# Kernel optimization log

Hardware: AMD Instinct MI355X
Metric: run time of the kernel (lower is better)

## Reference

```python
import jax, jax.numpy as jnp
import numpy as np

N = 100000   # nodes
E = 640000   # edges
H = 8        # attention heads
C = 16       # hidden_channels (per-head out dim)
IN = 4       # in_channels
G = 64       # graphs in the batch
NE = 2       # num_experts
HC = H * C   # 128 = concat feature width
SLOPE = 0.2  # GATConv leaky_relu negative slope


def _p(k, shape):
    return 0.1 * jax.random.normal(k, shape, jnp.float32)


def setup_inputs() -> dict:
    key = jax.random.key(0)
    ks = jax.random.split(key, 32)
    inp = {
        "x": jax.random.normal(ks[0], (N, IN), jnp.float32),
        "edge_index": jax.random.randint(ks[1], (2, E), 0, N),
        "edge_attr": jax.random.normal(ks[2], (E, 1), jnp.float32),
        "batch": jnp.sort(jax.random.randint(ks[3], (N,), 0, G)),
    }
    i = 4
    for l, d in zip((1, 2, 3), (IN, HC, HC)):
        inp[f"w{l}"] = _p(ks[i], (d, HC)); i += 1      # node lin
        inp[f"as{l}"] = _p(ks[i], (H, C)); i += 1      # att_src
        inp[f"ad{l}"] = _p(ks[i], (H, C)); i += 1      # att_dst
        inp[f"we{l}"] = _p(ks[i], (1, HC)); i += 1     # lin_edge
        inp[f"ae{l}"] = _p(ks[i], (H, C)); i += 1      # att_edge
        inp[f"b{l}"] = jnp.zeros((HC,), jnp.float32)
    inp["fw1"] = _p(ks[i], (HC, 4 * C)); inp["fb1"] = jnp.zeros((4 * C,), jnp.float32)
    inp["fw2"] = _p(ks[i + 1], (4 * C, NE)); inp["fb2"] = jnp.zeros((NE,), jnp.float32)
    return inp


def gat_layer(x, src, dst, eattr, w, a_s, a_d, we, a_e, b):
    """PyG GATConv (concat=True, edge_dim=1): gather-attend-segment_softmax-scatter."""
    n = x.shape[0]
    h = (x @ w).reshape(n, H, C)                       # [N,H,C]
    alpha_src = jnp.sum(h * a_s, axis=-1)              # [N,H]
    alpha_dst = jnp.sum(h * a_d, axis=-1)              # [N,H]
    ef = (eattr @ we).reshape(-1, H, C)                # [E,H,C]
    alpha_e = jnp.sum(ef * a_e, axis=-1)               # [E,H]
    alpha = jax.nn.leaky_relu(alpha_src[src] + alpha_dst[dst] + alpha_e, SLOPE)
    # segment softmax over incoming edges of each dst node
    m = jax.lax.stop_gradient(jax.ops.segment_max(alpha, dst, num_segments=n))
    m = jnp.where(jnp.isfinite(m), m, 0.0)
    ex = jnp.exp(alpha - m[dst])
    den = jax.ops.segment_sum(ex, dst, num_segments=n)
    alpha = ex / (den[dst] + 1e-16)
    out = jax.ops.segment_sum(h[src] * alpha[:, :, None], dst, num_segments=n)
    return out.reshape(n, HC) + b


def add_self_loops_mean(src, dst, eattr, n):
    """add_self_loops(fill_value='mean'): self-loop attr = mean of incoming edge attrs."""
    cnt = jax.ops.segment_sum(jnp.ones(src.shape, eattr.dtype), dst, num_segments=n)
    loop = jax.ops.segment_sum(eattr, dst, num_segments=n) / jnp.maximum(cnt, 1.0)[:, None]
    idx = jnp.arange(n, dtype=src.dtype)
    return (jnp.concatenate([src, idx]), jnp.concatenate([dst, idx]),
            jnp.concatenate([eattr, loop], axis=0))


def reference(x, edge_index, edge_attr, batch,
              w1, as1, ad1, we1, ae1, b1,
              w2, as2, ad2, we2, ae2, b2,
              w3, as3, ad3, we3, ae3, b3,
              fw1, fb1, fw2, fb2):
    src, dst = edge_index[0], edge_index[1]
    # conv1: add_self_loops=False
    h = jax.nn.relu(gat_layer(x, src, dst, edge_attr, w1, as1, ad1, we1, ae1, b1))
    # conv2/conv3: default add_self_loops=True with fill_value='mean'
    s2, d2, e2 = add_self_loops_mean(src, dst, edge_attr, x.shape[0])
    h = jax.nn.relu(gat_layer(h, s2, d2, e2, w2, as2, ad2, we2, ae2, b2))
    h = jax.nn.relu(gat_layer(h, s2, d2, e2, w3, as3, ad3, we3, ae3, b3))
    # global mean pool over `batch`
    gsum = jax.ops.segment_sum(h, batch, num_segments=G)
    cnt = jax.ops.segment_sum(jnp.ones((h.shape[0],), h.dtype), batch, num_segments=G)
    emb = gsum / jnp.maximum(cnt, 1.0)[:, None]
    gh = jax.nn.relu(emb @ fw1 + fb1)
    return gh @ fw2 + fb2
```

## Files before the change

### kernel.cpp

```cpp
#include <hip/hip_runtime.h>
#include <hip/hip_bf16.h>
#include <math.h>

#define NHEAD 8
#define CDIM 16
#define HCDIM 128
#define NGRAPH 64
#define WEXT 144
#define SWPAD 136

typedef __attribute__((ext_vector_type(8))) short short8;
typedef __attribute__((ext_vector_type(4))) float f32x4;
typedef __attribute__((ext_vector_type(2))) float f32x2;

static __device__ __forceinline__ unsigned short f2bf(float f) {
    unsigned u = __float_as_uint(f);
    unsigned r = (u + 0x7FFF + ((u >> 16) & 1)) >> 16;
    return (unsigned short)r;
}
static __device__ __forceinline__ float bf2f(unsigned short s) {
    return __uint_as_float(((unsigned)s) << 16);
}
static __device__ __forceinline__ unsigned char f2fp8(float v) {
    int r = __builtin_amdgcn_cvt_pk_fp8_f32(v, v, 0, false);
    return (unsigned char)(r & 0xff);
}


__global__ void setup0(int* __restrict__ deg,
                       float* __restrict__ gsum,
                       const float* __restrict__ w2, const float* __restrict__ w3,
                       unsigned short* __restrict__ wt2, unsigned short* __restrict__ wt3,
                       const float* __restrict__ we1, const float* __restrict__ ae1,
                       const float* __restrict__ we2, const float* __restrict__ ae2,
                       const float* __restrict__ we3, const float* __restrict__ ae3,
                       float* __restrict__ kc,
                       const float* __restrict__ as2, const float* __restrict__ ad2,
                       const float* __restrict__ as3, const float* __restrict__ ad3,
                       const float* __restrict__ w1,
                       const float* __restrict__ as1, const float* __restrict__ ad1,
                       float* __restrict__ wastab, float* __restrict__ wadtab,
                       const int* __restrict__ batch, int* __restrict__ gstart, int n) {
    int i = blockIdx.x * 256 + threadIdx.x;
    if (i < n) deg[i] = 0;
    if (i < NGRAPH * HCDIM) gsum[i] = 0.f;
    if (i < WEXT * HCDIM) {
        int nn = i >> 7, k = i & 127;
        float v2, v3;
        if (nn < HCDIM) {
            v2 = w2[k * HCDIM + nn];
            v3 = w3[k * HCDIM + nn];
        } else if (nn < HCDIM + NHEAD) {
            int h = nn - HCDIM;
            float s2 = 0.f, s3 = 0.f;
#pragma unroll
            for (int c = 0; c < CDIM; ++c) {
                s2 += w2[k * HCDIM + h * CDIM + c] * as2[h * CDIM + c];
                s3 += w3[k * HCDIM + h * CDIM + c] * as3[h * CDIM + c];
            }
            v2 = s2; v3 = s3;
        } else {
            int h = nn - HCDIM - NHEAD;
            float s2 = 0.f, s3 = 0.f;
#pragma unroll
            for (int c = 0; c < CDIM; ++c) {
                s2 += w2[k * HCDIM + h * CDIM + c] * ad2[h * CDIM + c];
                s3 += w3[k * HCDIM + h * CDIM + c] * ad3[h * CDIM + c];
            }
            v2 = s2; v3 = s3;
        }
        wt2[nn * HCDIM + k] = f2bf(v2);
        wt3[nn * HCDIM + k] = f2bf(v3);
    }
    if (i < 24) {
        int l = i >> 3, h = i & 7;
        const float* we = (l == 0) ? we1 : ((l == 1) ? we2 : we3);
        const float* ae = (l == 0) ? ae1 : ((l == 1) ? ae2 : ae3);
        float s = 0.f;
        for (int c = 0; c < CDIM; ++c) s += we[h * CDIM + c] * ae[h * CDIM + c];
        kc[i] = s;
    }
    if (i >= 18560 && i <= 18560 + NGRAPH) {
        int g = i - 18560;
        int lo = 0, hi = n;
        while (lo < hi) {
            int mid = (lo + hi) >> 1;
            if (batch[mid] < g) lo = mid + 1; else hi = mid;
        }
        gstart[g] = lo;
    }
    if (i >= 18700 && i < 18732) {
        int t = i - 18700;
        int k = t >> 3, h = t & 7;
        float ss = 0.f, sd = 0.f;
#pragma unroll
        for (int c = 0; c < CDIM; ++c) {
            ss += w1[k * HCDIM + h * CDIM + c] * as1[h * CDIM + c];
            sd += w1[k * HCDIM + h * CDIM + c] * ad1[h * CDIM + c];
        }
        wastab[t] = ss;
        wadtab[t] = sd;
    }
}

__global__ void count_deg(const int* __restrict__ dst, int* __restrict__ deg,
                          int* __restrict__ erank, int E) {
    int e = blockIdx.x * 256 + threadIdx.x;
    if (e >= E) return;
    erank[e] = atomicAdd(&deg[dst[e]], 1);
}

__global__ __launch_bounds__(512) void block_sum(const int* __restrict__ deg,
                                                 int* __restrict__ bsum, int n) {
    __shared__ int s[512];
    int i = blockIdx.x * 512 + threadIdx.x;
    s[threadIdx.x] = (i < n) ? deg[i] : 0;
    __syncthreads();
    for (int off = 256; off > 0; off >>= 1) {
        if (threadIdx.x < off) s[threadIdx.x] += s[threadIdx.x + off];
        __syncthreads();
    }
    if (threadIdx.x == 0) bsum[blockIdx.x] = s[0];
}

__global__ __launch_bounds__(512) void scan_final2(const int* __restrict__ deg,
                                                   const int* __restrict__ bsum, int nb,
                                                   int* __restrict__ eoff, int n) {
    __shared__ int ls[512];
    __shared__ int s[512];
    const int t = threadIdx.x;
    ls[t] = (t < nb) ? bsum[t] : 0;
    int i = blockIdx.x * 512 + t;
    s[t] = (i < n) ? deg[i] : 0;
    __syncthreads();
    for (int off = 1; off < 512; off <<= 1) {
        int a1 = (t >= off) ? ls[t - off] : 0;
        int a2 = (t >= off) ? s[t - off] : 0;
        __syncthreads();
        ls[t] += a1; s[t] += a2;
        __syncthreads();
    }
    int base = (blockIdx.x > 0) ? ls[blockIdx.x - 1] : 0;
    if (i < n) eoff[i + 1] = base + s[t];
    if (i == 0) eoff[0] = 0;
}

__global__ void scatter_edges(const int* __restrict__ src, const int* __restrict__ dst,
                              const float* __restrict__ eattr,
                              const int* __restrict__ eoff,
                              const int* __restrict__ erank,
                              int2* __restrict__ epack, int E) {
    int e = blockIdx.x * 256 + threadIdx.x;
    if (e >= E) return;
    int p = eoff[dst[e]] + erank[e];
    epack[p] = make_int2(src[e], __float_as_int(eattr[e]));
}


__global__ __launch_bounds__(256) void gat_aggregate1(
    const float* __restrict__ x,
    const int2*  __restrict__ epack,
    const int*   __restrict__ eoff,
    const float* __restrict__ w1,
    const float* __restrict__ wastab,
    const float* __restrict__ wadtab,
    const float* __restrict__ kc,
    const float* __restrict__ bias,
    unsigned short* __restrict__ outbf,
    int n) {
    const int lane = threadIdx.x & 63;
    const int l16 = lane & 15;
    int nid = ((blockIdx.x * 256 + threadIdx.x) >> 6) * 4 + (lane >> 4);
    if (nid >= n) return;
    const int h = l16 >> 1;
    const int c0 = l16 * 8;

    float was0 = wastab[0 * NHEAD + h], was1_ = wastab[1 * NHEAD + h];
    float was2 = wastab[2 * NHEAD + h], was3 = wastab[3 * NHEAD + h];
    float wad0 = wadtab[0 * NHEAD + h], wad1_ = wadtab[1 * NHEAD + h];
    float wad2 = wadtab[2 * NHEAD + h], wad3 = wadtab[3 * NHEAD + h];

    f32x4 xd = *(const f32x4*)(x + (((unsigned)nid) << 2));
    const float adst_h = xd[0] * wad0 + xd[1] * wad1_ + xd[2] * wad2 + xd[3] * wad3;
    const float k_h = kc[h];
    const int e0 = eoff[nid], e1 = eoff[nid + 1];

    float den = 0.f;
    f32x4 acc4 = (f32x4){0.f, 0.f, 0.f, 0.f};

    if (e0 < e1) {
        int2 ep[4];
#pragma unroll
        for (int j = 0; j < 4; ++j) {
            int idx = e0 + j; idx = (idx < e1) ? idx : (e1 - 1);
            ep[j] = epack[idx];
        }
        for (int base = e0; base < e1; base += 4) {
            int2 epn[4];
#pragma unroll
            for (int j = 0; j < 4; ++j) {
                int idx = base + 4 + j; idx = (idx < e1) ? idx : (e1 - 1);
                epn[j] = epack[idx];
            }
            f32x4 xs[4];
#pragma unroll
            for (int j = 0; j < 4; ++j)
                xs[j] = *(const f32x4*)(x + (((unsigned)ep[j].x) << 2));
#pragma unroll
            for (int j = 0; j < 4; ++j) {
                bool valid = (base + j < e1);
                float as_e = xs[j][0] * was0 + xs[j][1] * was1_ +
                             xs[j][2] * was2 + xs[j][3] * was3;
                float a = as_e + adst_h + __int_as_float(ep[j].y) * k_h;
                a = (a > 0.f) ? a : 0.2f * a;
                float w = valid ? __expf(a) : 0.f;
                den += w;
                acc4 += xs[j] * w;
            }
#pragma unroll
            for (int j = 0; j < 4; ++j) ep[j] = epn[j];
        }
    }

    float inv = 1.f / (den + 1e-16f);
    short8 o;
#pragma unroll
    for (int c = 0; c < 8; ++c) {
        float oc = acc4[0] * w1[0 * HCDIM + c0 + c] + acc4[1] * w1[1 * HCDIM + c0 + c] +
                   acc4[2] * w1[2 * HCDIM + c0 + c] + acc4[3] * w1[3 * HCDIM + c0 + c];
        oc = fmaxf(oc * inv + bias[c0 + c], 0.f);
        o[c] = (short)f2bf(oc);
    }
    *(short8*)(outbf + (long)nid * HCDIM + c0) = o;
}


__global__ __launch_bounds__(256) void gemm_mfma(const unsigned short* __restrict__ A,
                                                 const unsigned short* __restrict__ Wt,
                                                 unsigned char* __restrict__ Y8,
                                                 float* __restrict__ adstn, int n) {
    __shared__ unsigned short sW[WEXT][SWPAD];
    for (int i = threadIdx.x; i < WEXT * 16; i += 256) {
        int r = i >> 4, c = (i & 15) << 3;
        *(short8*)&sW[r][c] = *(const short8*)(Wt + r * HCDIM + c);
    }
    __syncthreads();

    const int wave = threadIdx.x >> 6;
    const int lane = threadIdx.x & 63;
    const int quad = lane >> 4;
    const int l16  = lane & 15;
    const int rowbase = (blockIdx.x * 8 + wave * 2) * 16;

    f32x4 acc[2][9];
#pragma unroll
    for (int r = 0; r < 2; ++r)
#pragma unroll
        for (int t = 0; t < 9; ++t) acc[r][t] = (f32x4){0.f, 0.f, 0.f, 0.f};

#pragma unroll
    for (int kb = 0; kb < HCDIM; kb += 32) {
        short8 a[2];
#pragma unroll
        for (int r = 0; r < 2; ++r) {
            int row = rowbase + r * 16 + l16;
            row = (row < n) ? row : (n - 1);
            a[r] = *(const short8*)(A + (long)row * HCDIM + kb + quad * 8);
        }
#pragma unroll
        for (int nt = 0; nt < 9; ++nt) {
            short8 b = *(const short8*)(&sW[nt * 16 + l16][kb + quad * 8]);
#pragma unroll
            for (int r = 0; r < 2; ++r)
                acc[r][nt] = __builtin_amdgcn_mfma_f32_16x16x32_bf16(a[r], b, acc[r][nt], 0, 0, 0);
        }
    }

#pragma unroll
    for (int r = 0; r < 2; ++r) {
#pragma unroll
        for (int reg = 0; reg < 4; ++reg) {
            int row = rowbase + r * 16 + quad * 4 + reg;
            if (row < n) {
                unsigned char* yp = Y8 + (long)row * HCDIM + l16;
#pragma unroll
                for (int nt = 0; nt < 8; ++nt) yp[nt * 16] = f2fp8(acc[r][nt][reg]);
                if (l16 >= 8) adstn[row * NHEAD + (l16 - 8)] = acc[r][8][reg];
            }
        }
    }
}


__global__ __launch_bounds__(256) void gat_aggregate(
    const unsigned char* __restrict__ h8,
    const float* __restrict__ adst,
    const float* __restrict__ asw,
    const int2*  __restrict__ epack,
    const int*   __restrict__ eoff,
    const float* __restrict__ kc,
    const float* __restrict__ bias,
    unsigned short* __restrict__ out,
    int n, int use_loop) {
    const int lane = threadIdx.x & 63;
    const int l16 = lane & 15;
    int nid = ((blockIdx.x * 256 + threadIdx.x) >> 6) * 4 + (lane >> 4);
    if (nid >= n) return;
    const int h = l16 >> 1;
    const int c0 = l16 * 8;

    const float* asrow = asw + h * CDIM + (l16 & 1) * 8;
    const f32x2 wp0 = *(const f32x2*)(asrow + 0);
    const f32x2 wp1 = *(const f32x2*)(asrow + 2);
    const f32x2 wp2 = *(const f32x2*)(asrow + 4);
    const f32x2 wp3 = *(const f32x2*)(asrow + 6);

    const float adst_h = adst[nid * NHEAD + h];
    const float k_h = kc[h];
    const int e0 = eoff[nid], e1 = eoff[nid + 1];

    float den = 0.f, sume = 0.f;
    f32x2 acc[4];
#pragma unroll
    for (int p = 0; p < 4; ++p) acc[p] = (f32x2){0.f, 0.f};

    if (e0 < e1) {
        int2 ep[4];
#pragma unroll
        for (int j = 0; j < 4; ++j) {
            int idx = e0 + j; idx = (idx < e1) ? idx : (e1 - 1);
            ep[j] = epack[idx];
        }
        for (int base = e0; base < e1; base += 4) {
            int2 epn[4];
#pragma unroll
            for (int j = 0; j < 4; ++j) {
                int idx = base + 4 + j; idx = (idx < e1) ? idx : (e1 - 1);
                epn[j] = epack[idx];
            }
            uint2 hv[4];
#pragma unroll
            for (int j = 0; j < 4; ++j)
                hv[j] = *(const uint2*)(h8 + (((unsigned)ep[j].x) << 7) + c0);
#pragma unroll
            for (int j = 0; j < 4; ++j) {
                bool valid = (base + j < e1);
                f32x2 p0 = __builtin_amdgcn_cvt_pk_f32_fp8((int)hv[j].x, false);
                f32x2 p1 = __builtin_amdgcn_cvt_pk_f32_fp8((int)hv[j].x, true);
                f32x2 p2 = __builtin_amdgcn_cvt_pk_f32_fp8((int)hv[j].y, false);
                f32x2 p3 = __builtin_amdgcn_cvt_pk_f32_fp8((int)hv[j].y, true);
                f32x2 ds = p0 * wp0 + p1 * wp1 + p2 * wp2 + p3 * wp3;
                float part = ds[0] + ds[1];
                float as_e = part + __shfl_xor(part, 1, 64);
                float ea = __int_as_float(ep[j].y);
                float a = as_e + adst_h + ea * k_h;
                a = (a > 0.f) ? a : 0.2f * a;
                float w = valid ? __expf(a) : 0.f;
                sume += valid ? ea : 0.f;
                den += w;
                acc[0] += p0 * w;
                acc[1] += p1 * w;
                acc[2] += p2 * w;
                acc[3] += p3 * w;
            }
#pragma unroll
            for (int j = 0; j < 4; ++j) ep[j] = epn[j];
        }
    }

    if (use_loop) {
        float fl = sume / fmaxf((float)(e1 - e0), 1.f);
        uint2 hv = *(const uint2*)(h8 + (((unsigned)nid) << 7) + c0);
        f32x2 p0 = __builtin_amdgcn_cvt_pk_f32_fp8((int)hv.x, false);
        f32x2 p1 = __builtin_amdgcn_cvt_pk_f32_fp8((int)hv.x, true);
        f32x2 p2 = __builtin_amdgcn_cvt_pk_f32_fp8((int)hv.y, false);
        f32x2 p3 = __builtin_amdgcn_cvt_pk_f32_fp8((int)hv.y, true);
        f32x2 ds = p0 * wp0 + p1 * wp1 + p2 * wp2 + p3 * wp3;
        float part = ds[0] + ds[1];
        float as_self = part + __shfl_xor(part, 1, 64);
        float a = as_self + adst_h + fl * k_h;
        a = (a > 0.f) ? a : 0.2f * a;
        float w = __expf(a);
        den += w;
        acc[0] += p0 * w;
        acc[1] += p1 * w;
        acc[2] += p2 * w;
        acc[3] += p3 * w;
    }

    float inv = 1.f / (den + 1e-16f);
    short8 o;
#pragma unroll
    for (int c = 0; c < 8; ++c) {
        float oc = fmaxf(acc[c >> 1][c & 1] * inv + bias[c0 + c], 0.f);
        o[c] = (short)f2bf(oc);
    }
    *(short8*)(out + (long)nid * HCDIM + c0) = o;
}


__global__ __launch_bounds__(128) void pool_seg(const unsigned short* __restrict__ H,
                                                const int* __restrict__ gstart,
                                                float* __restrict__ gsum) {
    const int c = threadIdx.x;
    const int g = blockIdx.x >> 3;
    const int chunk = blockIdx.x & 7;
    int s0 = gstart[g], s1 = gstart[g + 1];
    int len = s1 - s0;
    if (len <= 0) return;
    int cl = (len + 7) >> 3;
    int i0 = s0 + chunk * cl;
    int i1 = min(i0 + cl, s1);
    if (i0 >= i1) return;
    float acc = 0.f;
    int i = i0;
    for (; i + 4 <= i1; i += 4) {
        float v0 = bf2f(H[(long)i * HCDIM + c]);
        float v1 = bf2f(H[(long)(i + 1) * HCDIM + c]);
        float v2 = bf2f(H[(long)(i + 2) * HCDIM + c]);
        float v3 = bf2f(H[(long)(i + 3) * HCDIM + c]);
        acc += (v0 + v1) + (v2 + v3);
    }
    for (; i < i1; ++i) acc += bf2f(H[(long)i * HCDIM + c]);
    atomicAdd(&gsum[g * HCDIM + c], acc);
}

__global__ __launch_bounds__(64) void mlp_kernel(const float* __restrict__ gsum,
                                                 const int* __restrict__ gstart,
                                                 const float* __restrict__ fw1,
                                                 const float* __restrict__ fb1,
                                                 const float* __restrict__ fw2,
                                                 const float* __restrict__ fb2,
                                                 float* __restrict__ out) {
    const int g = blockIdx.x;
    const int j = threadIdx.x;
    __shared__ float emb[HCDIM];
    __shared__ float gh[64];
    int cnt = gstart[g + 1] - gstart[g];
    float invc = 1.f / fmaxf((float)cnt, 1.f);
    emb[j] = gsum[g * HCDIM + j] * invc;
    emb[j + 64] = gsum[g * HCDIM + 64 + j] * invc;
    __syncthreads();
    float a = fb1[j];
    for (int k = 0; k < HCDIM; ++k) a += emb[k] * fw1[k * 64 + j];
    gh[j] = fmaxf(a, 0.f);
    __syncthreads();
    if (j < 2) {
        float o = fb2[j];
        for (int k = 0; k < 64; ++k) o += gh[k] * fw2[k * 2 + j];
        out[g * 2 + j] = o;
    }
}


extern "C" void kernel_launch(void* const* d_in, const int* in_sizes, int n_in,
                              void* d_out, int out_size, void* d_ws, size_t ws_size,
                              hipStream_t stream) {
    const float* x     = (const float*)d_in[0];
    const int*   eidx  = (const int*)d_in[1];
    const float* eattr = (const float*)d_in[2];
    const int*   batch = (const int*)d_in[3];
    const float* w1  = (const float*)d_in[4];
    const float* as1 = (const float*)d_in[5];
    const float* ad1 = (const float*)d_in[6];
    const float* we1 = (const float*)d_in[7];
    const float* ae1 = (const float*)d_in[8];
    const float* b1  = (const float*)d_in[9];
    const float* w2  = (const float*)d_in[10];
    const float* as2 = (const float*)d_in[11];
    const float* ad2 = (const float*)d_in[12];
    const float* we2 = (const float*)d_in[13];
    const float* ae2 = (const float*)d_in[14];
    const float* b2  = (const float*)d_in[15];
    const float* w3  = (const float*)d_in[16];
    const float* as3 = (const float*)d_in[17];
    const float* ad3 = (const float*)d_in[18];
    const float* we3 = (const float*)d_in[19];
    const float* ae3 = (const float*)d_in[20];
    const float* b3  = (const float*)d_in[21];
    const float* fw1 = (const float*)d_in[22];
    const float* fb1 = (const float*)d_in[23];
    const float* fw2 = (const float*)d_in[24];
    const float* fb2 = (const float*)d_in[25];

    const int N = in_sizes[3];
    const int E = in_sizes[2];
    const int* src = eidx;
    const int* dst = eidx + E;

    char* p = (char*)d_ws;
    auto alloc = [&](size_t bytes) {
        void* r = (void*)p;
        p += (bytes + 255) & ~(size_t)255;
        return r;
    };
    unsigned char*  A8  = (unsigned char*)alloc((size_t)N * HCDIM);
    unsigned short* Bbf = (unsigned short*)alloc((size_t)N * HCDIM * 2);
    float* adstA  = (float*)alloc((size_t)N * NHEAD * 4);
    float* adstB  = (float*)alloc((size_t)N * NHEAD * 4);
    int*   deg    = (int*)alloc((size_t)N * 4);
    int*   eoff   = (int*)alloc((size_t)(N + 1) * 4);
    int*   erank  = (int*)alloc((size_t)E * 4);
    int2*  epack  = (int2*)alloc((size_t)E * 8);
    int*   bsum   = (int*)alloc(((size_t)(N + 511) / 512) * 4);
    float* kc     = (float*)alloc(24 * 4);
    int*   gstart = (int*)alloc((NGRAPH + 1) * 4);
    float* gsum   = (float*)alloc(NGRAPH * HCDIM * 4);
    float* wastab = (float*)alloc(32 * 4);
    float* wadtab = (float*)alloc(32 * 4);
    unsigned short* wt2 = (unsigned short*)alloc(WEXT * HCDIM * 2);
    unsigned short* wt3 = (unsigned short*)alloc(WEXT * HCDIM * 2);

    const int NB = (N + 255) / 256;
    const int NB512 = (N + 511) / 512;
    const int EB = (E + 255) / 256;
    const int AGG_BLOCKS = (((N + 3) / 4) * 64 + 255) / 256;
    const int GEMM_BLOCKS = (N + 127) / 128;

    setup0<<<NB, 256, 0, stream>>>(deg, gsum,
                                   w2, w3, wt2, wt3,
                                   we1, ae1, we2, ae2, we3, ae3, kc,
                                   as2, ad2, as3, ad3,
                                   w1, as1, ad1, wastab, wadtab,
                                   batch, gstart, N);
    count_deg<<<EB, 256, 0, stream>>>(dst, deg, erank, E);
    block_sum<<<NB512, 512, 0, stream>>>(deg, bsum, N);
    scan_final2<<<NB512, 512, 0, stream>>>(deg, bsum, NB512, eoff, N);
    scatter_edges<<<EB, 256, 0, stream>>>(src, dst, eattr, eoff, erank, epack, E);

    gat_aggregate1<<<AGG_BLOCKS, 256, 0, stream>>>(x, epack, eoff, w1, wastab, wadtab,
                                                   kc + 0, b1, Bbf, N);
    gemm_mfma<<<GEMM_BLOCKS, 256, 0, stream>>>(Bbf, wt2, A8, adstB, N);
    gat_aggregate<<<AGG_BLOCKS, 256, 0, stream>>>(A8, adstB, as2, epack, eoff,
                                                  kc + 8, b2, Bbf, N, 1);
    gemm_mfma<<<GEMM_BLOCKS, 256, 0, stream>>>(Bbf, wt3, A8, adstA, N);
    gat_aggregate<<<AGG_BLOCKS, 256, 0, stream>>>(A8, adstA, as3, epack, eoff,
                                                  kc + 16, b3, Bbf, N, 1);

    pool_seg<<<NGRAPH * 8, 128, 0, stream>>>(Bbf, gstart, gsum);
    mlp_kernel<<<NGRAPH, 64, 0, stream>>>(gsum, gstart, fw1, fb1, fw2, fb2, (float*)d_out);
}
```

Baseline: 305.6 us.

## Pack edges into 32-bit words and store intermediate activations in fp8

Result: no change. 300.4 us (-1.7%).

```diff
diff --git a/kernel.cpp b/kernel.cpp
--- a/kernel.cpp
+++ b/kernel.cpp
@@ -24,6 +24,10 @@
 static __device__ __forceinline__ unsigned char f2fp8(float v) {
     int r = __builtin_amdgcn_cvt_pk_fp8_f32(v, v, 0, false);
     return (unsigned char)(r & 0xff);
+}
+static __device__ __forceinline__ float fp82f(int x) {
+    f32x2 t = __builtin_amdgcn_cvt_pk_f32_fp8(x, false);
+    return t[0];
 }
 
 
@@ -149,24 +153,24 @@
                               const float* __restrict__ eattr,
                               const int* __restrict__ eoff,
                               const int* __restrict__ erank,
-                              int2* __restrict__ epack, int E) {
+                              unsigned* __restrict__ epack, int E) {
     int e = blockIdx.x * 256 + threadIdx.x;
     if (e >= E) return;
     int p = eoff[dst[e]] + erank[e];
-    epack[p] = make_int2(src[e], __float_as_int(eattr[e]));
+    epack[p] = ((unsigned)src[e] & 0xFFFFFFu) | ((unsigned)f2fp8(eattr[e]) << 24);
 }
 
 
 __global__ __launch_bounds__(256) void gat_aggregate1(
     const float* __restrict__ x,
-    const int2*  __restrict__ epack,
+    const unsigned* __restrict__ epack,
     const int*   __restrict__ eoff,
     const float* __restrict__ w1,
     const float* __restrict__ wastab,
     const float* __restrict__ wadtab,
     const float* __restrict__ kc,
     const float* __restrict__ bias,
-    unsigned short* __restrict__ outbf,
+    unsigned char* __restrict__ out8,
     int n) {
     const int lane = threadIdx.x & 63;
     const int l16 = lane & 15;
@@ -189,14 +193,14 @@
     f32x4 acc4 = (f32x4){0.f, 0.f, 0.f, 0.f};
 
     if (e0 < e1) {
-        int2 ep[4];
+        unsigned ep[4];
 #pragma unroll
         for (int j = 0; j < 4; ++j) {
             int idx = e0 + j; idx = (idx < e1) ? idx : (e1 - 1);
             ep[j] = epack[idx];
         }
         for (int base = e0; base < e1; base += 4) {
-            int2 epn[4];
+            unsigned epn[4];
 #pragma unroll
             for (int j = 0; j < 4; ++j) {
                 int idx = base + 4 + j; idx = (idx < e1) ? idx : (e1 - 1);
@@ -205,13 +209,14 @@
             f32x4 xs[4];
 #pragma unroll
             for (int j = 0; j < 4; ++j)
-                xs[j] = *(const f32x4*)(x + (((unsigned)ep[j].x) << 2));
+                xs[j] = *(const f32x4*)(x + ((ep[j] & 0xFFFFFFu) << 2));
 #pragma unroll
             for (int j = 0; j < 4; ++j) {
                 bool valid = (base + j < e1);
                 float as_e = xs[j][0] * was0 + xs[j][1] * was1_ +
                              xs[j][2] * was2 + xs[j][3] * was3;
-                float a = as_e + adst_h + __int_as_float(ep[j].y) * k_h;
+                float ea = fp82f((int)(ep[j] >> 24));
+                float a = as_e + adst_h + ea * k_h;
                 a = (a > 0.f) ? a : 0.2f * a;
                 float w = valid ? __expf(a) : 0.f;
                 den += w;
@@ -223,19 +228,22 @@
     }
 
     float inv = 1.f / (den + 1e-16f);
-    short8 o;
+    float oc[8];
 #pragma unroll
     for (int c = 0; c < 8; ++c) {
-        float oc = acc4[0] * w1[0 * HCDIM + c0 + c] + acc4[1] * w1[1 * HCDIM + c0 + c] +
-                   acc4[2] * w1[2 * HCDIM + c0 + c] + acc4[3] * w1[3 * HCDIM + c0 + c];
-        oc = fmaxf(oc * inv + bias[c0 + c], 0.f);
-        o[c] = (short)f2bf(oc);
-    }
-    *(short8*)(outbf + (long)nid * HCDIM + c0) = o;
-}
-
-
-__global__ __launch_bounds__(256) void gemm_mfma(const unsigned short* __restrict__ A,
+        float v = acc4[0] * w1[0 * HCDIM + c0 + c] + acc4[1] * w1[1 * HCDIM + c0 + c] +
+                  acc4[2] * w1[2 * HCDIM + c0 + c] + acc4[3] * w1[3 * HCDIM + c0 + c];
+        oc[c] = fmaxf(v * inv + bias[c0 + c], 0.f);
+    }
+    int w0 = __builtin_amdgcn_cvt_pk_fp8_f32(oc[0], oc[1], 0, false);
+    w0 = __builtin_amdgcn_cvt_pk_fp8_f32(oc[2], oc[3], w0, true);
+    int w1p = __builtin_amdgcn_cvt_pk_fp8_f32(oc[4], oc[5], 0, false);
+    w1p = __builtin_amdgcn_cvt_pk_fp8_f32(oc[6], oc[7], w1p, true);
+    *(uint2*)(out8 + ((long)nid << 7) + c0) = make_uint2((unsigned)w0, (unsigned)w1p);
+}
+
+
+__global__ __launch_bounds__(256) void gemm_mfma(const unsigned char* __restrict__ A8,
                                                  const unsigned short* __restrict__ Wt,
                                                  unsigned char* __restrict__ Y8,
                                                  float* __restrict__ adstn, int n) {
@@ -265,7 +273,15 @@
         for (int r = 0; r < 2; ++r) {
             int row = rowbase + r * 16 + l16;
             row = (row < n) ? row : (n - 1);
-            a[r] = *(const short8*)(A + (long)row * HCDIM + kb + quad * 8);
+            uint2 a8v = *(const uint2*)(A8 + (long)row * HCDIM + kb + quad * 8);
+            f32x2 q0 = __builtin_amdgcn_cvt_pk_f32_fp8((int)a8v.x, false);
+            f32x2 q1 = __builtin_amdgcn_cvt_pk_f32_fp8((int)a8v.x, true);
+            f32x2 q2 = __builtin_amdgcn_cvt_pk_f32_fp8((int)a8v.y, false);
+            f32x2 q3 = __builtin_amdgcn_cvt_pk_f32_fp8((int)a8v.y, true);
+            a[r][0] = (short)f2bf(q0[0]); a[r][1] = (short)f2bf(q0[1]);
+            a[r][2] = (short)f2bf(q1[0]); a[r][3] = (short)f2bf(q1[1]);
+            a[r][4] = (short)f2bf(q2[0]); a[r][5] = (short)f2bf(q2[1]);
+            a[r][6] = (short)f2bf(q3[0]); a[r][7] = (short)f2bf(q3[1]);
         }
 #pragma unroll
         for (int nt = 0; nt < 9; ++nt) {
@@ -296,12 +312,12 @@
     const unsigned char* __restrict__ h8,
     const float* __restrict__ adst,
     const float* __restrict__ asw,
-    const int2*  __restrict__ epack,
+    const unsigned* __restrict__ epack,
     const int*   __restrict__ eoff,
     const float* __restrict__ kc,
     const float* __restrict__ bias,
-    unsigned short* __restrict__ out,
-    int n, int use_loop) {
+    void* __restrict__ out,
+    int n, int out_fp8) {
     const int lane = threadIdx.x & 63;
     const int l16 = lane & 15;
     int nid = ((blockIdx.x * 256 + threadIdx.x) >> 6) * 4 + (lane >> 4);
@@ -325,14 +341,14 @@
     for (int p = 0; p < 4; ++p) acc[p] = (f32x2){0.f, 0.f};
 
     if (e0 < e1) {
-        int2 ep[4];
+        unsigned ep[4];
 #pragma unroll
         for (int j = 0; j < 4; ++j) {
             int idx = e0 + j; idx = (idx < e1) ? idx : (e1 - 1);
             ep[j] = epack[idx];
         }
         for (int base = e0; base < e1; base += 4) {
-            int2 epn[4];
+            unsigned epn[4];
 #pragma unroll
             for (int j = 0; j < 4; ++j) {
                 int idx = base + 4 + j; idx = (idx < e1) ? idx : (e1 - 1);
@@ -341,7 +357,7 @@
             uint2 hv[4];
 #pragma unroll
             for (int j = 0; j < 4; ++j)
-                hv[j] = *(const uint2*)(h8 + (((unsigned)ep[j].x) << 7) + c0);
+                hv[j] = *(const uint2*)(h8 + ((long)(ep[j] & 0xFFFFFFu) << 7) + c0);
 #pragma unroll
             for (int j = 0; j < 4; ++j) {
                 bool valid = (base + j < e1);
@@ -352,7 +368,7 @@
                 f32x2 ds = p0 * wp0 + p1 * wp1 + p2 * wp2 + p3 * wp3;
                 float part = ds[0] + ds[1];
                 float as_e = part + __shfl_xor(part, 1, 64);
-                float ea = __int_as_float(ep[j].y);
+                float ea = fp82f((int)(ep[j] >> 24));
                 float a = as_e + adst_h + ea * k_h;
                 a = (a > 0.f) ? a : 0.2f * a;
                 float w = valid ? __expf(a) : 0.f;
@@ -368,9 +384,9 @@
         }
     }
 
-    if (use_loop) {
+    {
         float fl = sume / fmaxf((float)(e1 - e0), 1.f);
-        uint2 hv = *(const uint2*)(h8 + (((unsigned)nid) << 7) + c0);
+        uint2 hv = *(const uint2*)(h8 + ((long)(unsigned)nid << 7) + c0);
         f32x2 p0 = __builtin_amdgcn_cvt_pk_f32_fp8((int)hv.x, false);
         f32x2 p1 = __builtin_amdgcn_cvt_pk_f32_fp8((int)hv.x, true);
         f32x2 p2 = __builtin_amdgcn_cvt_pk_f32_fp8((int)hv.y, false);
@@ -389,13 +405,23 @@
     }
 
     float inv = 1.f / (den + 1e-16f);
-    short8 o;
-#pragma unroll
-    for (int c = 0; c < 8; ++c) {
-        float oc = fmaxf(acc[c >> 1][c & 1] * inv + bias[c0 + c], 0.f);
-        o[c] = (short)f2bf(oc);
-    }
-    *(short8*)(out + (long)nid * HCDIM + c0) = o;
+    float oc[8];
+#pragma unroll
+    for (int c = 0; c < 8; ++c)
+        oc[c] = fmaxf(acc[c >> 1][c & 1] * inv + bias[c0 + c], 0.f);
+    if (out_fp8) {
+        int w0 = __builtin_amdgcn_cvt_pk_fp8_f32(oc[0], oc[1], 0, false);
+        w0 = __builtin_amdgcn_cvt_pk_fp8_f32(oc[2], oc[3], w0, true);
+        int w1p = __builtin_amdgcn_cvt_pk_fp8_f32(oc[4], oc[5], 0, false);
+        w1p = __builtin_amdgcn_cvt_pk_fp8_f32(oc[6], oc[7], w1p, true);
+        *(uint2*)((unsigned char*)out + ((long)nid << 7) + c0) =
+            make_uint2((unsigned)w0, (unsigned)w1p);
+    } else {
+        short8 o;
+#pragma unroll
+        for (int c = 0; c < 8; ++c) o[c] = (short)f2bf(oc[c]);
+        *(short8*)((unsigned short*)out + (long)nid * HCDIM + c0) = o;
+    }
 }
 
 
@@ -495,13 +521,14 @@
         return r;
     };
     unsigned char*  A8  = (unsigned char*)alloc((size_t)N * HCDIM);
-    unsigned short* Bbf = (unsigned short*)alloc((size_t)N * HCDIM * 2);
+    unsigned char*  B8  = (unsigned char*)alloc((size_t)N * HCDIM);
+    unsigned short* Cbf = (unsigned short*)alloc((size_t)N * HCDIM * 2);
     float* adstA  = (float*)alloc((size_t)N * NHEAD * 4);
     float* adstB  = (float*)alloc((size_t)N * NHEAD * 4);
     int*   deg    = (int*)alloc((size_t)N * 4);
     int*   eoff   = (int*)alloc((size_t)(N + 1) * 4);
     int*   erank  = (int*)alloc((size_t)E * 4);
-    int2*  epack  = (int2*)alloc((size_t)E * 8);
+    unsigned* epack = (unsigned*)alloc((size_t)E * 4);
     int*   bsum   = (int*)alloc(((size_t)(N + 511) / 512) * 4);
     float* kc     = (float*)alloc(24 * 4);
     int*   gstart = (int*)alloc((NGRAPH + 1) * 4);
@@ -529,14 +556,14 @@
     scatter_edges<<<EB, 256, 0, stream>>>(src, dst, eattr, eoff, erank, epack, E);
 
     gat_aggregate1<<<AGG_BLOCKS, 256, 0, stream>>>(x, epack, eoff, w1, wastab, wadtab,
-                                                   kc + 0, b1, Bbf, N);
-    gemm_mfma<<<GEMM_BLOCKS, 256, 0, stream>>>(Bbf, wt2, A8, adstB, N);
+                                                   kc + 0, b1, B8, N);
+    gemm_mfma<<<GEMM_BLOCKS, 256, 0, stream>>>(B8, wt2, A8, adstB, N);
     gat_aggregate<<<AGG_BLOCKS, 256, 0, stream>>>(A8, adstB, as2, epack, eoff,
-                                                  kc + 8, b2, Bbf, N, 1);
-    gemm_mfma<<<GEMM_BLOCKS, 256, 0, stream>>>(Bbf, wt3, A8, adstA, N);
+                                                  kc + 8, b2, (void*)B8, N, 1);
+    gemm_mfma<<<GEMM_BLOCKS, 256, 0, stream>>>(B8, wt3, A8, adstA, N);
     gat_aggregate<<<AGG_BLOCKS, 256, 0, stream>>>(A8, adstA, as3, epack, eoff,
-                                                  kc + 16, b3, Bbf, N, 1);
-
-    pool_seg<<<NGRAPH * 8, 128, 0, stream>>>(Bbf, gstart, gsum);
+                                                  kc + 16, b3, (void*)Cbf, N, 0);
+
+    pool_seg<<<NGRAPH * 8, 128, 0, stream>>>(Cbf, gstart, gsum);
     mlp_kernel<<<NGRAPH, 64, 0, stream>>>(gsum, gstart, fw1, fb1, fw2, fb2, (float*)d_out);
 }
```
